# Kernel optimization log

Hardware: AMD Instinct MI355X
Metric: run time of the kernel (lower is better)

The kernel has to match this reference:

```python
import jax, jax.numpy as jnp
import numpy as np

CROP = (96.0, 192.0, 192.0)
SPACING = jnp.array([2.0, 1.0, 1.0], dtype=jnp.float32)
TOPK = 7
IGNORE_RATIO = 26
ALPHA, GAMMA = 0.75, 2.0
RATIO, NUM_HARD = 100, 100


def make_anchors(D, H, W):
    zz, yy, xx = jnp.meshgrid(jnp.arange(D, dtype=jnp.float32),
                              jnp.arange(H, dtype=jnp.float32),
                              jnp.arange(W, dtype=jnp.float32), indexing='ij')
    anchors = jnp.stack([zz, yy, xx], -1).reshape(-1, 3)  # [A,3] (z,y,x), z-major like cartesian_prod
    stride = jnp.array([CROP[0] / D, CROP[1] / H, CROP[2] / W], dtype=jnp.float32)
    return anchors, stride


def target_preprocess(ann):
    # ann [B,N,7] = (cz,cy,cx,d,h,w,label); clip boxes to the crop, keep boxes with
    c, s, label = ann[..., 0:3], ann[..., 3:6], ann[..., 6]
    has_box = label > -1
    lo = jnp.maximum(c - s / 2, 0.0)
    hi = jnp.minimum(c + s / 2, jnp.array(CROP, dtype=ann.dtype))
    n = jnp.clip(hi - lo, 0.0)
    vol = n[..., 0] * n[..., 1] * n[..., 2]
    percent = vol / (s[..., 0] * s[..., 1] * s[..., 2])
    good = (percent > 0.1) & (vol >= 15.0)
    keep = has_box & (vol > 0) & good
    rejected = has_box & (vol > 0) & (~good)
    new_box = jnp.concatenate([lo + n / 2, n, jnp.zeros_like(label)[..., None]], -1)
    ann_new = jnp.where(keep[..., None], new_box, -1.0)
    return ann_new, lo, hi, rejected


def build_grid_ignore(lo, hi, rejected, D, H, W):
    # Faithful to original: image-space coords index the feature grid directly,
    # with python-slice clipping emulated by the < / >= comparisons.
    def axis_mask(a0, a1, L):
        idx = jnp.arange(L, dtype=jnp.float32)
        return (idx >= jnp.floor(a0)[..., None]) & (idx < jnp.ceil(a1)[..., None])
    mz = axis_mask(lo[..., 0], hi[..., 0], D)  # [B,N,D]
    my = axis_mask(lo[..., 1], hi[..., 1], H)
    mx = axis_mask(lo[..., 2], hi[..., 2], W)
    region = (rejected[..., None, None, None] & mz[:, :, :, None, None]
              & my[:, :, None, :, None] & mx[:, :, None, None, :])
    return -jnp.any(region, axis=1).astype(jnp.float32)  # [B,D,H,W], 0 or -1


def scatter_count(inds, A):
    # one_hot(inds).sum(-2) without materializing [B,N,K,A]
    B, N, K = inds.shape
    bi = jnp.arange(B)[:, None, None]
    ni = jnp.arange(N)[None, :, None]
    return jnp.zeros((B, N, A), jnp.float32).at[bi, ni, inds].add(1.0)


def get_pos_target(ann, anchors, stride):
    B, N, _ = ann.shape
    A = anchors.shape[0]
    mask_gt = (ann[..., -1] > -1).astype(jnp.float32)  # [B,N]
    ctr = ann[..., :3] / stride
    half = ann[..., 3:6] / 2
    dist = -(((ctr[:, :, None, :] - anchors[None, None]) * SPACING) ** 2).sum(-1)  # [B,N,A]
    _, inds = jax.lax.top_k(dist, (IGNORE_RATIO + 1) * TOPK)
    mask_topk = scatter_count(inds[..., :TOPK], A)
    mask_ign = -scatter_count(inds[..., TOPK:], A)
    mask_pos = mask_topk * mask_gt[..., None]
    mask_ign = mask_ign * mask_gt[..., None]
    gt_idx = jnp.argmax(mask_pos, axis=1) + jnp.arange(B)[:, None] * N  # [B,A]
    t_ctr = ctr.reshape(-1, 3)[gt_idx]
    t_offset = t_ctr - anchors[None]
    t_shape = half.reshape(-1, 3)[gt_idx]
    t_bboxes = ann[..., :6].reshape(-1, 6)[gt_idx]
    t_scores = mask_pos.max(axis=1)[..., None]   # [B,A,1]
    m_ignore = mask_ign.min(axis=1)[..., None]
    return t_offset, t_shape, t_bboxes, t_scores, m_ignore


def bbox_diou(box1, box2, eps=1e-7):
    c1, s1 = box1[..., :3], box1[..., 3:]
    c2, s2 = box2[..., :3], box2[..., 3:]
    lo1, hi1 = c1 - s1 / 2, c1 + s1 / 2
    lo2, hi2 = c2 - s2 / 2, c2 + s2 / 2
    inter = jnp.clip(jnp.minimum(hi1, hi2) - jnp.maximum(lo1, lo2), 0.0).prod(-1) + eps
    union = s1.prod(-1) + s2.prod(-1) - inter
    iou = inter / union
    c2d = ((jnp.maximum(hi1, hi2) - jnp.minimum(lo1, lo2)) ** 2).sum(-1) + eps
    rho2 = (((lo2 + hi2) - (lo1 + hi1)) ** 2).sum(-1) / 4
    return iou - rho2 / c2d


def focal_cls_loss(pred, target, ignore):
    # pred/target/ignore: [B,A]. Hard-negative mining: top (100*num_pos) negatives
    # (or top 100 when no positives) via a rank mask over the descending sort.
    prob = jnp.clip(jax.nn.sigmoid(jax.lax.stop_gradient(pred)), 1e-4, 1.0 - 1e-4)
    is_pos = target == 1.0
    alpha_f = jnp.where(is_pos, ALPHA, 1.0 - ALPHA)
    fw = alpha_f * jnp.where(is_pos, 1.0 - prob, prob) ** GAMMA
    bce = jnp.logaddexp(0.0, pred) - pred * target  # BCE-with-logits, stable
    loss = jnp.where(ignore == 0, fw * bce, 0.0)
    loss = jnp.where((prob < 0.8) & is_pos, 4.0 * loss, loss)  # FN up-weighting
    npos = is_pos.sum(axis=1)
    pos_sum = jnp.where(is_pos, loss, 0.0).sum(axis=1)
    neg = jnp.where(target == 0.0, loss, -1.0)
    neg_sorted = jnp.flip(jnp.sort(neg, axis=1), axis=1)
    k = jnp.where(npos > 0, RATIO * npos, NUM_HARD)
    ranks = jnp.arange(neg.shape[1])[None, :]
    neg_sum = jnp.where((ranks < k[:, None]) & (neg_sorted >= 0), neg_sorted, 0.0).sum(axis=1)
    per_img = (pos_sum + neg_sum) / jnp.maximum(npos.astype(pred.dtype), 1.0)
    return per_img.mean()


def detection_loss(cls_out, shape_out, offset_out, annotations):
    B = cls_out.shape[0]
    D, H, W = cls_out.shape[2:]
    anchors, stride = make_anchors(D, H, W)
    pred_scores = cls_out.reshape(B, -1)                       # [B,A]
    pred_shapes = shape_out.reshape(B, 3, -1).transpose(0, 2, 1)   # [B,A,3]
    pred_offsets = offset_out.reshape(B, 3, -1).transpose(0, 2, 1)
    ann_new, lo, hi, rejected = target_preprocess(annotations)
    grid_ign = build_grid_ignore(lo, hi, rejected, D, H, W).reshape(B, -1)  # [B,A]
    pred_bboxes = jnp.concatenate([(anchors + pred_offsets) * stride, 2 * pred_shapes], -1)
    t_off, t_shape, t_bbox, t_scores, m_ign = get_pos_target(ann_new, anchors, stride)
    cls_l = focal_cls_loss(pred_scores, t_scores[..., 0], m_ign[..., 0] + grid_ign)
    fg = (t_scores[..., 0] == 1.0).astype(cls_out.dtype)  # [B,A]
    denom = jnp.maximum(fg.sum(), 1.0)
    shape_l = (jnp.abs(pred_shapes - t_shape) * fg[..., None]).sum() / (denom * 3)
    off_l = (jnp.abs(pred_offsets - t_off) * fg[..., None]).sum() / (denom * 3)
    iou_l = 1.0 - (bbox_diou(pred_bboxes, t_bbox) * fg).sum() / denom
    return cls_l, shape_l, off_l, iou_l


def setup_inputs() -> dict:
    key = jax.random.key(0)
    k1, k2, k3, k4, k5, k6 = jax.random.split(key, 6)
    B, N = 16, 8
    D, H, W = 24, 48, 48
    cls_out = jax.random.normal(k1, (B, 1, D, H, W), jnp.float32)
    shape_out = jax.random.uniform(k2, (B, 3, D, H, W), jnp.float32) * 4.0 + 1.0
    offset_out = jax.random.normal(k3, (B, 3, D, H, W), jnp.float32) * 0.5
    crop = jnp.array(CROP)
    ctr = jax.random.uniform(k4, (B, N, 3)) * (crop - 16.0) + 8.0
    size = jax.random.uniform(k5, (B, N, 3)) * 16.0 + 6.0
    size = size.at[:, 1, :].set(2.0)      # vol=8 < 15 -> rejected -> exercises ignore path
    ctr = ctr.at[:, 0, 0].set(3.0)        # near z=0 edge -> clipping path
    valid = jax.random.uniform(k6, (B, N)) < 0.6
    label = jnp.where(valid, 0.0, -1.0)
    annotations = jnp.where(valid[..., None],
                            jnp.concatenate([ctr, size, label[..., None]], -1), -1.0)
    return {"cls_out": cls_out, "shape_out": shape_out,
            "offset_out": offset_out, "annotations": annotations}


def reference(cls_out, shape_out, offset_out, annotations):
    return detection_loss(cls_out, shape_out, offset_out, annotations)
```

## Files before the change

### kernel.cpp

```cpp
#include <hip/hip_runtime.h>

#define BB 16
#define NN 8
#define DD 24
#define HH 48
#define WW 48
#define AA (DD*HH*WW)
#define AW (AA/32)
#define NSEG (AA/256)
#define TOPKc 7
#define KIGN 189
#define NB1 2048
#define DCAP 16384

#define WZC 13
#define WYC 25
#define WXC 25
#define WYXC (WYC*WXC)
#define CNTC (WZC*WYXC)
#define CPT 32

struct GT {
  float ctr[3];
  float half_[3];
  float bbox[6];
  float lo[3], hi[3];
  int keep, rejected;
};

struct Accum {
  int   npos[BB];
  float pos_sum[BB];
  float shape_sum, off_sum, iou_sum;
  int   B1[BB];
  int   cnt_above[BB];
  float per_img[BB];
};

__device__ __forceinline__ unsigned fkey(float f) {
  unsigned u = __float_as_uint(f);
  return (u & 0x80000000u) ? ~u : (u | 0x80000000u);
}
__device__ __forceinline__ float fkey_inv(unsigned k) {
  return __uint_as_float((k & 0x80000000u) ? (k & 0x7FFFFFFFu) : ~k);
}

__device__ __forceinline__ void agg_lds_add(int* h, int bin) {
  const int lane = threadIdx.x & 63;
  unsigned long long todo = __ballot(bin >= 0);
  while (todo) {
    const int leader = __ffsll((unsigned long long)todo) - 1;
    const int lbin = __shfl(bin, leader, 64);
    const unsigned long long eq = __ballot(bin == lbin) & todo;
    if (lane == leader) atomicAdd(&h[lbin], (int)__popcll(eq));
    todo &= ~eq;
  }
}

__device__ __forceinline__ GT prep_gt(const float* __restrict__ p) {
  const float cz=p[0], cy=p[1], cx=p[2], sz=p[3], sy=p[4], sx=p[5], label=p[6];
  const bool has_box = label > -1.0f;
  const float loz = fmaxf(cz - sz*0.5f, 0.0f);
  const float loy = fmaxf(cy - sy*0.5f, 0.0f);
  const float lox = fmaxf(cx - sx*0.5f, 0.0f);
  const float hiz = fminf(cz + sz*0.5f, 96.0f);
  const float hiy = fminf(cy + sy*0.5f, 192.0f);
  const float hix = fminf(cx + sx*0.5f, 192.0f);
  const float nz = fmaxf(hiz - loz, 0.0f);
  const float ny = fmaxf(hiy - loy, 0.0f);
  const float nx = fmaxf(hix - lox, 0.0f);
  const float vol = nz * ny * nx;
  const float percent = vol / (sz * sy * sx);
  const bool good = (percent > 0.1f) && (vol >= 15.0f);
  const bool keep = has_box && (vol > 0.0f) && good;
  const bool rejected = has_box && (vol > 0.0f) && !good;
  GT g;
  const float ncz = loz + nz*0.5f, ncy = loy + ny*0.5f, ncx = lox + nx*0.5f;
  if (keep) {
    g.ctr[0]=ncz*0.25f; g.ctr[1]=ncy*0.25f; g.ctr[2]=ncx*0.25f;
    g.half_[0]=nz*0.5f; g.half_[1]=ny*0.5f; g.half_[2]=nx*0.5f;
    g.bbox[0]=ncz; g.bbox[1]=ncy; g.bbox[2]=ncx;
    g.bbox[3]=nz;  g.bbox[4]=ny;  g.bbox[5]=nx;
  } else {
    for (int j=0;j<3;++j){ g.ctr[j]=-0.25f; g.half_[j]=-0.5f; }
    for (int j=0;j<6;++j) g.bbox[j]=-1.0f;
  }
  g.lo[0]=loz; g.lo[1]=loy; g.lo[2]=lox;
  g.hi[0]=hiz; g.hi[1]=hiy; g.hi[2]=hix;
  g.keep = keep ? 1 : 0;
  g.rejected = rejected ? 1 : 0;
  return g;
}

__device__ __forceinline__ int blockReduceSumI(int v) {
  __shared__ int s[4];
  for (int off = 32; off; off >>= 1) v += __shfl_down(v, off, 64);
  if ((threadIdx.x & 63) == 0) s[threadIdx.x >> 6] = v;
  __syncthreads();
  int r = s[0] + s[1] + s[2] + s[3];
  __syncthreads();
  return r;
}
__device__ __forceinline__ float blockReduceSumF(float v) {
  __shared__ float s[4];
  for (int off = 32; off; off >>= 1) v += __shfl_down(v, off, 64);
  if ((threadIdx.x & 63) == 0) s[threadIdx.x >> 6] = v;
  __syncthreads();
  float r = s[0] + s[1] + s[2] + s[3];
  __syncthreads();
  return r;
}
__device__ __forceinline__ int redI1024(int v) {
  __shared__ int s[16];
  for (int off = 32; off; off >>= 1) v += __shfl_down(v, off, 64);
  if ((threadIdx.x & 63) == 0) s[threadIdx.x >> 6] = v;
  __syncthreads();
  int r = 0;
  #pragma unroll
  for (int w = 0; w < 16; ++w) r += s[w];
  __syncthreads();
  return r;
}
__device__ __forceinline__ float redF1024(float v) {
  __shared__ float s[16];
  for (int off = 32; off; off >>= 1) v += __shfl_down(v, off, 64);
  if ((threadIdx.x & 63) == 0) s[threadIdx.x >> 6] = v;
  __syncthreads();
  float r = 0.0f;
  #pragma unroll
  for (int w = 0; w < 16; ++w) r += s[w];
  __syncthreads();
  return r;
}

__device__ void suffix_find_1024(const int* h, int nbins, int ktarget,
                                 int* s_bin, int* s_cnt) {
  const int tid = threadIdx.x, lane = tid & 63, wave = tid >> 6;
  const int C = nbins >> 10;
  int csum = 0;
  for (int i = 0; i < C; ++i) csum += h[tid*C + i];
  __shared__ int wt[16];
  int S = csum;
  #pragma unroll
  for (int off = 1; off < 64; off <<= 1) {
    const int t = __shfl_down(S, off, 64);
    if (lane + off < 64) S += t;
  }
  if (lane == 0) wt[wave] = S;
  __syncthreads();
  int above = 0;
  for (int w = wave + 1; w < 16; ++w) above += wt[w];
  const int sfx = above + (S - csum);
  if (sfx < ktarget && sfx + csum >= ktarget) {
    int running = sfx;
    for (int i = C - 1; i >= 0; --i) {
      const int c = h[tid*C + i];
      if (running + c >= ktarget) { *s_bin = tid*C + i; *s_cnt = running; break; }
      running += c;
    }
  }
  __syncthreads();
}

__device__ __forceinline__ float seg_load(const float* lb, const int* pfi,
                                          const int* cn, int i) {
  int lo = 0, hi = NSEG - 1;
  while (lo < hi) { const int mid = (lo + hi) >> 1; if (pfi[mid] > i) hi = mid; else lo = mid + 1; }
  return lb[lo*256 + (i - (pfi[lo] - cn[lo]))];
}

#define N_POS4  (BB*AA/4)
#define N_IGN4  (BB*AW/4)
#define N_HIST4 (BB*NB1/4)

__global__ __launch_bounds__(256) void k0_init(int4* pos_n4, uint4* ign4,
                                               int4* hist4, Accum* acc) {
  const int idx = blockIdx.x*256 + threadIdx.x;
  if (idx < N_POS4) {
    pos_n4[idx] = make_int4(0x7FFFFFFF,0x7FFFFFFF,0x7FFFFFFF,0x7FFFFFFF);
  } else if (idx < N_POS4 + N_IGN4) {
    ign4[idx - N_POS4] = make_uint4(0,0,0,0);
  } else if (idx < N_POS4 + N_IGN4 + N_HIST4) {
    hist4[idx - (N_POS4 + N_IGN4)] = make_int4(0,0,0,0);
  }
  if (idx < BB) {
    acc->npos[idx] = 0; acc->pos_sum[idx] = 0.0f;
    acc->B1[idx] = 0; acc->cnt_above[idx] = 0;
  }
  if (idx == 0) { acc->shape_sum = 0.0f; acc->off_sum = 0.0f; acc->iou_sum = 0.0f; }
}

__global__ __launch_bounds__(256) void k2_topk(const float* __restrict__ ann,
                                               int* __restrict__ pos_n,
                                               unsigned* __restrict__ ign) {
  const int bn = blockIdx.x;
  const int b = bn >> 3, n = bn & 7;
  const GT g = prep_gt(ann + bn*7);
  if (!g.keep) return;
  const float cz = g.ctr[0], cy = g.ctr[1], cx = g.ctr[2];
  const int rz = (int)floorf(cz + 0.5f);
  const int ry = (int)floorf(cy + 0.5f);
  const int rx = (int)floorf(cx + 0.5f);
  const int zlo = min(max(rz - 6, 0),  DD - WZC);
  const int ylo = min(max(ry - 12, 0), HH - WYC);
  const int xlo = min(max(rx - 12, 0), WW - WXC);
  const int tid = threadIdx.x;

  __shared__ int h[1024];
  #pragma unroll
  for (int i = 0; i < 4; ++i) h[tid + i*256] = 0;
  __syncthreads();

#define K2_KEYAID(J, KEY, AID, VALID)                                   \
  const int ci = tid + (J)*256;                                         \
  const bool VALID = ci < CNTC;                                         \
  const int wz = ci / WYXC;                                             \
  const int rem = ci - wz*WYXC;                                         \
  const int wy = rem / WXC;                                             \
  const int wx = rem - wy*WXC;                                          \
  const int z = zlo + wz, y = ylo + wy, x = xlo + wx;                   \
  const float dz = (cz - (float)z) * 2.0f;                              \
  const float dy = cy - (float)y;                                       \
  const float dx = cx - (float)x;                                      \
  const unsigned KEY = fkey(-__builtin_fmaf(dz, dz, __builtin_fmaf(dy, dy, dx*dx))); \
  const int AID = (z*HH + y)*WW + x;

  #pragma unroll
  for (int j = 0; j < CPT; ++j) {
    K2_KEYAID(j, key, aid, valid)
    (void)aid;
    if (valid) atomicAdd(&h[key >> 21], 1);
  }
  __syncthreads();

  __shared__ int wt[4];
  __shared__ int sB7, sA7, sB9, sA9;
  const int lane = tid & 63, wave = tid >> 6;
  int csum = 0;
  #pragma unroll
  for (int i = 0; i < 4; ++i) csum += h[tid*4 + i];
  int Ssc = csum;
  #pragma unroll
  for (int off = 1; off < 64; off <<= 1) {
    const int t = __shfl_down(Ssc, off, 64);
    if (lane + off < 64) Ssc += t;
  }
  if (lane == 0) wt[wave] = Ssc;
  __syncthreads();
  int above = 0;
  for (int w = wave + 1; w < 4; ++w) above += wt[w];
  const int sfx = above + (Ssc - csum);
  if (sfx < TOPKc && sfx + csum >= TOPKc) {
    int run = sfx;
    for (int i = 3; i >= 0; --i) {
      const int c = h[tid*4 + i];
      if (run + c >= TOPKc) { sB7 = tid*4 + i; sA7 = run; break; }
      run += c;
    }
  }
  if (sfx < KIGN && sfx + csum >= KIGN) {
    int run = sfx;
    for (int i = 3; i >= 0; --i) {
      const int c = h[tid*4 + i];
      if (run + c >= KIGN) { sB9 = tid*4 + i; sA9 = run; break; }
      run += c;
    }
  }
  __syncthreads();
  const int B7 = sB7, A7 = sA7, B9 = sB9, A9 = sA9;

  __shared__ unsigned kl7[512], kl9[512];
  __shared__ int n7s, n9s;
  if (tid == 0) { n7s = 0; n9s = 0; }
  __syncthreads();
  #pragma unroll
  for (int j = 0; j < CPT; ++j) {
    K2_KEYAID(j, key, aid, valid)
    (void)aid;
    if (valid) {
      const int bin = (int)(key >> 21);
      if (bin == B7) { const int p = atomicAdd(&n7s, 1); if (p < 512) kl7[p] = key; }
      if (bin == B9 && B9 != B7) { const int p = atomicAdd(&n9s, 1); if (p < 512) kl9[p] = key; }
    }
  }
  __syncthreads();

  __shared__ unsigned sk7, sk9;
  __shared__ int scg7, scg9;
  const int T7c = min(n7s, 512), T9c = min(n9s, 512);
  for (int i = tid; i < T7c; i += 256) {
    const unsigned xv = kl7[i];
    int gt = 0, eq = 0;
    for (int j2 = 0; j2 < T7c; ++j2) { gt += (kl7[j2] > xv); eq += (kl7[j2] == xv); }
    if (A7 + gt < TOPKc && TOPKc <= A7 + gt + eq) { sk7 = xv; scg7 = A7 + gt; }
    if (B9 == B7 && A7 + gt < KIGN && KIGN <= A7 + gt + eq) { sk9 = xv; scg9 = A7 + gt; }
  }
  if (B9 != B7) {
    for (int i = tid; i < T9c; i += 256) {
      const unsigned xv = kl9[i];
      int gt = 0, eq = 0;
      for (int j2 = 0; j2 < T9c; ++j2) { gt += (kl9[j2] > xv); eq += (kl9[j2] == xv); }
      if (A9 + gt < KIGN && KIGN <= A9 + gt + eq) { sk9 = xv; scg9 = A9 + gt; }
    }
  }
  __syncthreads();
  const unsigned k7 = sk7, k9 = sk9;
  const int cg7 = scg7, cg9 = scg9;

  __shared__ int tc7, tc9;
  __shared__ int tl7[256], tr7[256], tl9[256], tr9[256];
  if (tid == 0) { tc7 = 0; tc9 = 0; }
  __syncthreads();
  #pragma unroll
  for (int j = 0; j < CPT; ++j) {
    K2_KEYAID(j, key, aid, valid)
    if (valid) {
      if (key == k7) { const int p = atomicAdd(&tc7, 1); if (p < 256) tl7[p] = aid; }
      if (key == k9 && k9 != k7) { const int p = atomicAdd(&tc9, 1); if (p < 256) tl9[p] = aid; }
    }
  }
  __syncthreads();
  const int T7 = min(tc7, 256), T9 = min(tc9, 256);
  for (int i = tid; i < T7; i += 256) {
    const int ai = tl7[i]; int r = 0;
    for (int j2 = 0; j2 < T7; ++j2) r += (tl7[j2] < ai);
    tr7[i] = r;
  }
  for (int i = tid; i < T9; i += 256) {
    const int ai = tl9[i]; int r = 0;
    for (int j2 = 0; j2 < T9; ++j2) r += (tl9[j2] < ai);
    tr9[i] = r;
  }
  __syncthreads();

  int* pb = pos_n + (size_t)b*AA;
  unsigned* ib = ign + (size_t)b*AW;
  #pragma unroll
  for (int j = 0; j < CPT; ++j) {
    K2_KEYAID(j, key, aid, valid)
    if (valid) {
      bool top = false, igf = false;
      if (key > k7) top = true;
      else if (key == k7) {
        int r = 0;
        for (int t = 0; t < T7; ++t) if (tl7[t] == aid) r = tr7[t];
        const int ov = cg7 + r;
        if (ov < TOPKc) top = true;
        else if (ov < KIGN) igf = true;
      } else if (key > k9) igf = true;
      else if (key == k9) {
        int r = 0;
        for (int t = 0; t < T9; ++t) if (tl9[t] == aid) r = tr9[t];
        if (cg9 + r < KIGN) igf = true;
      }
      if (top) atomicMin(&pb[aid], n);
      else if (igf) atomicOr(&ib[aid >> 5], 1u << (aid & 31));
    }
  }
#undef K2_KEYAID
}

__global__ __launch_bounds__(256) void k3_loss(
    const float* __restrict__ cls_out, const float* __restrict__ shape_out,
    const float* __restrict__ offset_out, const float* __restrict__ ann,
    const int* __restrict__ pos_n, const unsigned* __restrict__ ignm,
    float* __restrict__ neg, int* __restrict__ ghist, Accum* acc) {
  __shared__ GT sg[NN];
  __shared__ int h1[NB1];
  const int idx = blockIdx.x * 256 + threadIdx.x;
  const int b = idx / AA;
  const int a = idx - b * AA;
  if (threadIdx.x < NN) sg[threadIdx.x] = prep_gt(ann + (b*NN + threadIdx.x)*7);
  #pragma unroll
  for (int i = 0; i < NB1/256; ++i) h1[threadIdx.x + i*256] = 0;
  __syncthreads();
  const int z = a / (HH*WW);
  const int rr = a - z*(HH*WW);
  const int y = rr / WW;
  const int x = rr - y*WW;

  float gign = 0.0f;
  for (int n = 0; n < NN; ++n) {
    if (!sg[n].rejected) continue;
    if ((float)z >= floorf(sg[n].lo[0]) && (float)z < ceilf(sg[n].hi[0]) &&
        (float)y >= floorf(sg[n].lo[1]) && (float)y < ceilf(sg[n].hi[1]) &&
        (float)x >= floorf(sg[n].lo[2]) && (float)x < ceilf(sg[n].hi[2])) gign = -1.0f;
  }

  const int pn = pos_n[idx];
  const bool is_pos = (pn < NN);
  const float target = is_pos ? 1.0f : 0.0f;
  const int ibit = (ignm[b*AW + (a >> 5)] >> (a & 31)) & 1;
  const float ignore = (ibit ? -1.0f : 0.0f) + gign;
  const float pred = cls_out[idx];
  float prob = 1.0f / (1.0f + expf(-pred));
  prob = fminf(fmaxf(prob, 1e-4f), 1.0f - 1e-4f);
  const float alpha_f = is_pos ? 0.75f : 0.25f;
  const float pt = is_pos ? (1.0f - prob) : prob;
  const float fw = alpha_f * pt * pt;
  const float bce = fmaxf(pred, 0.0f) + log1pf(expf(-fabsf(pred))) - pred * target;
  float loss = (ignore == 0.0f) ? fw * bce : 0.0f;
  if (prob < 0.8f && is_pos) loss *= 4.0f;
  const float nval = is_pos ? -1.0f : loss;
  neg[idx] = nval;

  agg_lds_add(h1, (int)(fkey(nval) >> 21));

  const int np = blockReduceSumI(is_pos ? 1 : 0);
  const float ps = blockReduceSumF(is_pos ? loss : 0.0f);
  if (threadIdx.x == 0 && np) {
    atomicAdd(&acc->npos[b], np);
    atomicAdd(&acc->pos_sum[b], ps);
  }

  if (is_pos) {
    const GT& g = sg[pn];
    const float toz = g.ctr[0] - (float)z;
    const float toy = g.ctr[1] - (float)y;
    const float tox = g.ctr[2] - (float)x;
    const float poz = offset_out[((size_t)b*3 + 0)*AA + a];
    const float poy = offset_out[((size_t)b*3 + 1)*AA + a];
    const float pox = offset_out[((size_t)b*3 + 2)*AA + a];
    const float psz = shape_out[((size_t)b*3 + 0)*AA + a];
    const float psy = shape_out[((size_t)b*3 + 1)*AA + a];
    const float psx = shape_out[((size_t)b*3 + 2)*AA + a];
    const float off_t = fabsf(poz - toz) + fabsf(poy - toy) + fabsf(pox - tox);
    const float shp_t = fabsf(psz - g.half_[0]) + fabsf(psy - g.half_[1]) + fabsf(psx - g.half_[2]);
    const float c1z = ((float)z + poz) * 4.0f;
    const float c1y = ((float)y + poy) * 4.0f;
    const float c1x = ((float)x + pox) * 4.0f;
    const float s1z = 2.0f*psz, s1y = 2.0f*psy, s1x = 2.0f*psx;
    const float lo1z = c1z - s1z*0.5f, hi1z = c1z + s1z*0.5f;
    const float lo1y = c1y - s1y*0.5f, hi1y = c1y + s1y*0.5f;
    const float lo1x = c1x - s1x*0.5f, hi1x = c1x + s1x*0.5f;
    const float c2z = g.bbox[0], c2y = g.bbox[1], c2x = g.bbox[2];
    const float s2z = g.bbox[3], s2y = g.bbox[4], s2x = g.bbox[5];
    const float lo2z = c2z - s2z*0.5f, hi2z = c2z + s2z*0.5f;
    const float lo2y = c2y - s2y*0.5f, hi2y = c2y + s2y*0.5f;
    const float lo2x = c2x - s2x*0.5f, hi2x = c2x + s2x*0.5f;
    const float iz = fmaxf(fminf(hi1z,hi2z) - fmaxf(lo1z,lo2z), 0.0f);
    const float iy = fmaxf(fminf(hi1y,hi2y) - fmaxf(lo1y,lo2y), 0.0f);
    const float ix = fmaxf(fminf(hi1x,hi2x) - fmaxf(lo1x,lo2x), 0.0f);
    const float inter = iz*iy*ix + 1e-7f;
    const float uni = s1z*s1y*s1x + s2z*s2y*s2x - inter;
    const float iou = inter / uni;
    const float ez = fmaxf(hi1z,hi2z) - fminf(lo1z,lo2z);
    const float ey = fmaxf(hi1y,hi2y) - fminf(lo1y,lo2y);
    const float ex = fmaxf(hi1x,hi2x) - fminf(lo1x,lo2x);
    const float c2d = (ez*ez + ey*ey) + ex*ex + 1e-7f;
    const float rz2 = (lo2z + hi2z) - (lo1z + hi1z);
    const float ry2 = (lo2y + hi2y) - (lo1y + hi1y);
    const float rx2 = (lo2x + hi2x) - (lo1x + hi1x);
    const float rho2 = ((rz2*rz2 + ry2*ry2) + rx2*rx2) * 0.25f;
    const float diou = iou - rho2 / c2d;
    atomicAdd(&acc->shape_sum, shp_t);
    atomicAdd(&acc->off_sum, off_t);
    atomicAdd(&acc->iou_sum, diou);
  }

  __syncthreads();
  #pragma unroll
  for (int i = 0; i < NB1/256; ++i) {
    const int bin = threadIdx.x + i*256;
    const int c = h1[bin];
    if (c) atomicAdd(&ghist[b*NB1 + bin], c);
  }
}

__global__ __launch_bounds__(256) void ks1(const int* __restrict__ ghist, Accum* acc) {
  const int b = blockIdx.x;
  const int* hb = ghist + b*NB1;
  const int tid = threadIdx.x, lane = tid & 63, wave = tid >> 6;
  const int npos = acc->npos[b];
  const int k = npos > 0 ? 100*npos : 100;
  int csum = 0;
  #pragma unroll
  for (int i = 0; i < 8; ++i) csum += hb[tid*8 + i];
  __shared__ int wt[4];
  int S = csum;
  #pragma unroll
  for (int off = 1; off < 64; off <<= 1) {
    const int t = __shfl_down(S, off, 64);
    if (lane + off < 64) S += t;
  }
  if (lane == 0) wt[wave] = S;
  __syncthreads();
  int above = 0;
  for (int w = wave + 1; w < 4; ++w) above += wt[w];
  const int sfx = above + (S - csum);
  if (sfx < k && sfx + csum >= k) {
    int running = sfx;
    for (int i = 7; i >= 0; --i) {
      const int c = hb[tid*8 + i];
      if (running + c >= k) {
        acc->B1[b] = tid*8 + i;
        acc->cnt_above[b] = running;
        break;
      }
      running += c;
    }
  }
}

__global__ __launch_bounds__(256) void kgather(const float* __restrict__ neg,
                                               float* __restrict__ list,
                                               float* __restrict__ psum,
                                               int* __restrict__ seg_cnt,
                                               const Accum* __restrict__ acc) {
  const int idx = blockIdx.x*256 + threadIdx.x;
  const int b = idx / AA;
  const int seg = (idx - b*AA) >> 8;
  const int tid = threadIdx.x, lane = tid & 63, wave = tid >> 6;
  const int B1 = acc->B1[b];
  const float val = neg[idx];
  const int bin = (int)(fkey(val) >> 21);
  const float aval = (bin > B1 && bin >= 1024) ? val : 0.0f;
  const float bs = blockReduceSumF(aval);

  const bool match = (bin == B1);
  const unsigned long long mask = __ballot(match);
  __shared__ int wc[4];
  if (lane == 0) wc[wave] = (int)__popcll(mask);
  __syncthreads();
  int wbase = 0;
  for (int w = 0; w < wave; ++w) wbase += wc[w];
  if (match) {
    const int pos = (int)__popcll(mask & ((1ull << lane) - 1ull));
    list[(size_t)b*AA + seg*256 + wbase + pos] = val;
  }
  if (tid == 0) {
    psum[b*NSEG + seg] = bs;
    seg_cnt[b*NSEG + seg] = wc[0] + wc[1] + wc[2] + wc[3];
  }
}

__global__ __launch_bounds__(1024) void ksel(const float* __restrict__ list,
                                             const float* __restrict__ psum,
                                             const int* __restrict__ seg_cnt,
                                             Accum* acc) {
  const int b = blockIdx.x;
  const int tid = threadIdx.x;
  const int npos = acc->npos[b];
  const int k = npos > 0 ? 100*npos : 100;
  const int B1 = acc->B1[b];
  const float pos_sum = acc->pos_sum[b];

  const float pv = (tid < NSEG) ? psum[b*NSEG + tid] : 0.0f;
  const float sum_above = redF1024(pv);

  if (B1 < 1024) {
    if (tid == 0) acc->per_img[b] = (pos_sum + sum_above) / fmaxf((float)npos, 1.0f);
    return;
  }

  __shared__ int cn[NSEG];
  __shared__ int pfi[256];
  if (tid < 256) {
    const int c = (tid < NSEG) ? seg_cnt[b*NSEG + tid] : 0;
    if (tid < NSEG) cn[tid] = c;
    pfi[tid] = c;
  }
  __syncthreads();
  for (int off = 1; off < 256; off <<= 1) {
    int v = 0;
    if (tid < 256 && tid >= off) v = pfi[tid - off];
    __syncthreads();
    if (tid < 256) pfi[tid] += v;
    __syncthreads();
  }
  const int S = pfi[NSEG - 1];
  const int cnt_above = acc->cnt_above[b];
  const int kt2 = k - cnt_above;
  const float* lb = list + (size_t)b*AA;

  __shared__ float ld[DCAP];
  const bool fits = (S <= DCAP);
  if (fits) {
    for (int i = tid; i < S; i += 1024) ld[i] = seg_load(lb, pfi, cn, i);
  }
  __syncthreads();

  __shared__ int h[2048];
  __shared__ int sB2, sC2, sB3, sC3;
  h[tid] = 0; h[tid + 1024] = 0;
  __syncthreads();
  for (int i0 = 0; i0 < S; i0 += 1024) {
    const int i = i0 + tid;
    if (i < S) {
      const float v = fits ? ld[i] : seg_load(lb, pfi, cn, i);
      atomicAdd(&h[(fkey(v) >> 10) & 0x7FF], 1);
    }
  }
  __syncthreads();
  suffix_find_1024(h, 2048, kt2, &sB2, &sC2);
  const int B2 = sB2;
  const int kt3 = kt2 - sC2;
  h[tid < 1024 ? tid : 0] = (tid < 1024) ? 0 : h[0];
  __syncthreads();
  float msum = 0.0f; int mcnt = 0;
  for (int i0 = 0; i0 < S; i0 += 1024) {
    const int i = i0 + tid;
    if (i < S) {
      const float v = fits ? ld[i] : seg_load(lb, pfi, cn, i);
      const unsigned key = fkey(v);
      const int sub = (int)((key >> 10) & 0x7FF);
      if (sub > B2) { msum += v; mcnt++; }
      else if (sub == B2) atomicAdd(&h[key & 0x3FF], 1);
    }
  }
  __syncthreads();
  suffix_find_1024(h, 1024, kt3, &sB3, &sC3);
  const int B3 = sB3;
  const unsigned Kstar = ((unsigned)B1 << 21) | ((unsigned)B2 << 10) | (unsigned)B3;
  const float v = fkey_inv(Kstar);
  for (int i0 = 0; i0 < S; i0 += 1024) {
    const int i = i0 + tid;
    if (i < S) {
      const float x = fits ? ld[i] : seg_load(lb, pfi, cn, i);
      const unsigned key = fkey(x);
      if ((int)((key >> 10) & 0x7FF) == B2 && (int)(key & 0x3FF) > B3) { msum += x; mcnt++; }
    }
  }
  const int cg = redI1024(mcnt);
  const float sg = redF1024(msum);
  if (tid == 0) {
    const int total_gt = cnt_above + cg;
    const float ns = sum_above + sg + (float)(k - total_gt) * v;
    acc->per_img[b] = (pos_sum + ns) / fmaxf((float)npos, 1.0f);
  }
}

__global__ void k5_final(const Accum* __restrict__ acc, float* __restrict__ out) {
  float s = 0.0f; int tot = 0;
  for (int b = 0; b < BB; ++b) { s += acc->per_img[b]; tot += acc->npos[b]; }
  out[0] = s / (float)BB;
  const float denom = fmaxf((float)tot, 1.0f);
  out[1] = acc->shape_sum / (denom * 3.0f);
  out[2] = acc->off_sum / (denom * 3.0f);
  out[3] = 1.0f - acc->iou_sum / denom;
}

extern "C" void kernel_launch(void* const* d_in, const int* in_sizes, int n_in,
                              void* d_out, int out_size, void* d_ws, size_t ws_size,
                              hipStream_t stream) {
  const float* cls_out    = (const float*)d_in[0];
  const float* shape_out  = (const float*)d_in[1];
  const float* offset_out = (const float*)d_in[2];
  const float* ann        = (const float*)d_in[3];
  float* out = (float*)d_out;

  char* ws = (char*)d_ws;
  Accum* acc    = (Accum*)ws;
  int* pos_n    = (int*)(ws + 1024);
  unsigned* ign = (unsigned*)(pos_n + (size_t)BB*AA);
  float* neg    = (float*)(ign + (size_t)BB*AW);
  int* ghist    = (int*)(neg + (size_t)BB*AA);
  float* psum   = (float*)(ghist + (size_t)BB*NB1);
  int* seg_cnt  = (int*)(psum + (size_t)BB*NSEG);
  float* list   = (float*)pos_n;

  const int n0 = N_POS4 + N_IGN4 + N_HIST4;
  hipLaunchKernelGGL(k0_init, dim3(n0/256), dim3(256), 0, stream,
                     (int4*)pos_n, (uint4*)ign, (int4*)ghist, acc);
  hipLaunchKernelGGL(k2_topk, dim3(BB*NN), dim3(256), 0, stream, ann, pos_n, ign);
  hipLaunchKernelGGL(k3_loss, dim3((BB*AA)/256), dim3(256), 0, stream,
                     cls_out, shape_out, offset_out, ann, pos_n, ign, neg, ghist, acc);
  hipLaunchKernelGGL(ks1, dim3(BB), dim3(256), 0, stream, ghist, acc);
  hipLaunchKernelGGL(kgather, dim3((BB*AA)/256), dim3(256), 0, stream,
                     neg, list, psum, seg_cnt, acc);
  hipLaunchKernelGGL(ksel, dim3(BB), dim3(1024), 0, stream, list, psum, seg_cnt, acc);
  hipLaunchKernelGGL(k5_final, dim3(1), dim3(1), 0, stream, acc, out);
}
```

Measured before the change: 69.60 us.

## Replace dense positive map with compact top-k lists and fold small kernels

Instead of a dense per-anchor int map initialised to sentinel and written with atomicMin, each GT now records its up-to-7 top-k anchors in a small list, and the loss kernel scans that 56-entry list from shared memory to decide positives. This removes a full BB*AA init write and read. The histogram threshold kernel ks1 is folded into each kgather block, which recomputes it redundantly. The final reduction k5 is folded into ksel through a last-block-done counter. Net effect is fewer launches and less memory traffic, at the cost of a 56-way compare per anchor and repeated histogram scans.

```diff
diff --git a/kernel.cpp b/kernel.cpp
--- a/kernel.cpp
+++ b/kernel.cpp
@@ -8,6 +8,7 @@
 #define AA (DD*HH*WW)
 #define AW (AA/32)
 #define NSEG (AA/256)
+#define NBLK ((BB*AA)/256)
 #define TOPKc 7
 #define KIGN 189
 #define NB1 2048
@@ -32,9 +33,11 @@
   int   npos[BB];
   float pos_sum[BB];
   float shape_sum, off_sum, iou_sum;
+  float sum_above[BB];
   int   B1[BB];
   int   cnt_above[BB];
   float per_img[BB];
+  int   done;
 };
 
 __device__ __forceinline__ unsigned fkey(float f) {
@@ -169,32 +172,22 @@
   return lb[lo*256 + (i - (pfi[lo] - cn[lo]))];
 }
 
-#define N_POS4  (BB*AA/4)
-#define N_IGN4  (BB*AW/4)
-#define N_HIST4 (BB*NB1/4)
-
-__global__ __launch_bounds__(256) void k0_init(int4* pos_n4, uint4* ign4,
-                                               int4* hist4, Accum* acc) {
+__global__ __launch_bounds__(256) void k0_init(unsigned* ign, int* ghist,
+                                               int* plist, Accum* acc) {
   const int idx = blockIdx.x*256 + threadIdx.x;
-  if (idx < N_POS4) {
-    pos_n4[idx] = make_int4(0x7FFFFFFF,0x7FFFFFFF,0x7FFFFFFF,0x7FFFFFFF);
-  } else if (idx < N_POS4 + N_IGN4) {
-    ign4[idx - N_POS4] = make_uint4(0,0,0,0);
-  } else if (idx < N_POS4 + N_IGN4 + N_HIST4) {
-    hist4[idx - (N_POS4 + N_IGN4)] = make_int4(0,0,0,0);
-  }
-  if (idx < BB) {
-    acc->npos[idx] = 0; acc->pos_sum[idx] = 0.0f;
-    acc->B1[idx] = 0; acc->cnt_above[idx] = 0;
-  }
-  if (idx == 0) { acc->shape_sum = 0.0f; acc->off_sum = 0.0f; acc->iou_sum = 0.0f; }
+  if (idx < BB*AW) ign[idx] = 0u;
+  const int i2 = idx - BB*AW;
+  if (i2 >= 0 && i2 < BB*NB1) ghist[i2] = 0;
+  const int i3 = idx - BB*AW - BB*NB1;
+  if (i3 >= 0 && i3 < BB*NN*TOPKc) plist[i3] = -1;
+  if (idx < (int)(sizeof(Accum)/4)) ((int*)acc)[idx] = 0;
 }
 
 __global__ __launch_bounds__(256) void k2_topk(const float* __restrict__ ann,
-                                               int* __restrict__ pos_n,
+                                               int* __restrict__ plist,
                                                unsigned* __restrict__ ign) {
   const int bn = blockIdx.x;
-  const int b = bn >> 3, n = bn & 7;
+  const int b = bn >> 3;
   const GT g = prep_gt(ann + bn*7);
   if (!g.keep) return;
   const float cz = g.ctr[0], cy = g.ctr[1], cx = g.ctr[2];
@@ -331,9 +324,10 @@
     for (int j2 = 0; j2 < T9; ++j2) r += (tl9[j2] < ai);
     tr9[i] = r;
   }
-  __syncthreads();
-
-  int* pb = pos_n + (size_t)b*AA;
+  __shared__ int pcnt;
+  if (tid == 0) pcnt = 0;
+  __syncthreads();
+
   unsigned* ib = ign + (size_t)b*AW;
   #pragma unroll
   for (int j = 0; j < CPT; ++j) {
@@ -353,7 +347,7 @@
         for (int t = 0; t < T9; ++t) if (tl9[t] == aid) r = tr9[t];
         if (cg9 + r < KIGN) igf = true;
       }
-      if (top) atomicMin(&pb[aid], n);
+      if (top) { const int s = atomicAdd(&pcnt, 1); if (s < TOPKc) plist[bn*TOPKc + s] = aid; }
       else if (igf) atomicOr(&ib[aid >> 5], 1u << (aid & 31));
     }
   }
@@ -363,14 +357,16 @@
 __global__ __launch_bounds__(256) void k3_loss(
     const float* __restrict__ cls_out, const float* __restrict__ shape_out,
     const float* __restrict__ offset_out, const float* __restrict__ ann,
-    const int* __restrict__ pos_n, const unsigned* __restrict__ ignm,
+    const int* __restrict__ plist, const unsigned* __restrict__ ignm,
     float* __restrict__ neg, int* __restrict__ ghist, Accum* acc) {
   __shared__ GT sg[NN];
+  __shared__ int pl[NN*TOPKc];
   __shared__ int h1[NB1];
   const int idx = blockIdx.x * 256 + threadIdx.x;
   const int b = idx / AA;
   const int a = idx - b * AA;
   if (threadIdx.x < NN) sg[threadIdx.x] = prep_gt(ann + (b*NN + threadIdx.x)*7);
+  if (threadIdx.x < NN*TOPKc) pl[threadIdx.x] = plist[b*NN*TOPKc + threadIdx.x];
   #pragma unroll
   for (int i = 0; i < NB1/256; ++i) h1[threadIdx.x + i*256] = 0;
   __syncthreads();
@@ -387,7 +383,9 @@
         (float)x >= floorf(sg[n].lo[2]) && (float)x < ceilf(sg[n].hi[2])) gign = -1.0f;
   }
 
-  const int pn = pos_n[idx];
+  int pn = NN;
+  #pragma unroll
+  for (int j = NN*TOPKc - 1; j >= 0; --j) if (pl[j] == a) pn = j / TOPKc;
   const bool is_pos = (pn < NN);
   const float target = is_pos ? 1.0f : 0.0f;
   const int ibit = (ignm[b*AW + (a >> 5)] >> (a & 31)) & 1;
@@ -467,51 +465,53 @@
   }
 }
 
-__global__ __launch_bounds__(256) void ks1(const int* __restrict__ ghist, Accum* acc) {
-  const int b = blockIdx.x;
-  const int* hb = ghist + b*NB1;
-  const int tid = threadIdx.x, lane = tid & 63, wave = tid >> 6;
-  const int npos = acc->npos[b];
-  const int k = npos > 0 ? 100*npos : 100;
-  int csum = 0;
-  #pragma unroll
-  for (int i = 0; i < 8; ++i) csum += hb[tid*8 + i];
-  __shared__ int wt[4];
-  int S = csum;
-  #pragma unroll
-  for (int off = 1; off < 64; off <<= 1) {
-    const int t = __shfl_down(S, off, 64);
-    if (lane + off < 64) S += t;
-  }
-  if (lane == 0) wt[wave] = S;
-  __syncthreads();
-  int above = 0;
-  for (int w = wave + 1; w < 4; ++w) above += wt[w];
-  const int sfx = above + (S - csum);
-  if (sfx < k && sfx + csum >= k) {
-    int running = sfx;
-    for (int i = 7; i >= 0; --i) {
-      const int c = hb[tid*8 + i];
-      if (running + c >= k) {
-        acc->B1[b] = tid*8 + i;
-        acc->cnt_above[b] = running;
-        break;
-      }
-      running += c;
-    }
-  }
-}
-
 __global__ __launch_bounds__(256) void kgather(const float* __restrict__ neg,
+                                               const int* __restrict__ ghist,
                                                float* __restrict__ list,
                                                float* __restrict__ psum,
                                                int* __restrict__ seg_cnt,
-                                               const Accum* __restrict__ acc) {
-  const int idx = blockIdx.x*256 + threadIdx.x;
-  const int b = idx / AA;
-  const int seg = (idx - b*AA) >> 8;
+                                               Accum* acc) {
+  const int bid = blockIdx.x;
   const int tid = threadIdx.x, lane = tid & 63, wave = tid >> 6;
-  const int B1 = acc->B1[b];
+  const int b = bid / NSEG;
+  const int seg = bid - b*NSEG;
+
+  const int npos = acc->npos[b];
+  const int k = npos > 0 ? 100*npos : 100;
+  __shared__ int sB1, sCA;
+  {
+    const int* hb = ghist + b*NB1;
+    int hv[8];
+    #pragma unroll
+    for (int i = 0; i < 8; ++i) hv[i] = hb[tid*8 + i];
+    int csum = 0;
+    #pragma unroll
+    for (int i = 0; i < 8; ++i) csum += hv[i];
+    __shared__ int wt[4];
+    int S = csum;
+    #pragma unroll
+    for (int off = 1; off < 64; off <<= 1) {
+      const int t = __shfl_down(S, off, 64);
+      if (lane + off < 64) S += t;
+    }
+    if (lane == 0) wt[wave] = S;
+    __syncthreads();
+    int above = 0;
+    for (int w = wave + 1; w < 4; ++w) above += wt[w];
+    const int sfx = above + (S - csum);
+    if (sfx < k && sfx + csum >= k) {
+      int run = sfx;
+      for (int i = 7; i >= 0; --i) {
+        if (run + hv[i] >= k) { sB1 = tid*8 + i; sCA = run; break; }
+        run += hv[i];
+      }
+    }
+    __syncthreads();
+  }
+  const int B1 = sB1, cnt_above = sCA;
+  if (seg == 0 && tid == 0) { acc->B1[b] = B1; acc->cnt_above[b] = cnt_above; }
+
+  const int idx = b*AA + seg*256 + tid;
   const float val = neg[idx];
   const int bin = (int)(fkey(val) >> 21);
   const float aval = (bin > B1 && bin >= 1024) ? val : 0.0f;
@@ -529,15 +529,15 @@
     list[(size_t)b*AA + seg*256 + wbase + pos] = val;
   }
   if (tid == 0) {
-    psum[b*NSEG + seg] = bs;
-    seg_cnt[b*NSEG + seg] = wc[0] + wc[1] + wc[2] + wc[3];
+    psum[bid] = bs;
+    seg_cnt[bid] = wc[0] + wc[1] + wc[2] + wc[3];
   }
 }
 
 __global__ __launch_bounds__(1024) void ksel(const float* __restrict__ list,
                                              const float* __restrict__ psum,
                                              const int* __restrict__ seg_cnt,
-                                             Accum* acc) {
+                                             Accum* acc, float* __restrict__ out) {
   const int b = blockIdx.x;
   const int tid = threadIdx.x;
   const int npos = acc->npos[b];
@@ -550,94 +550,99 @@
 
   if (B1 < 1024) {
     if (tid == 0) acc->per_img[b] = (pos_sum + sum_above) / fmaxf((float)npos, 1.0f);
-    return;
-  }
-
-  __shared__ int cn[NSEG];
-  __shared__ int pfi[256];
-  if (tid < 256) {
-    const int c = (tid < NSEG) ? seg_cnt[b*NSEG + tid] : 0;
-    if (tid < NSEG) cn[tid] = c;
-    pfi[tid] = c;
-  }
-  __syncthreads();
-  for (int off = 1; off < 256; off <<= 1) {
-    int v = 0;
-    if (tid < 256 && tid >= off) v = pfi[tid - off];
-    __syncthreads();
-    if (tid < 256) pfi[tid] += v;
-    __syncthreads();
-  }
-  const int S = pfi[NSEG - 1];
-  const int cnt_above = acc->cnt_above[b];
-  const int kt2 = k - cnt_above;
-  const float* lb = list + (size_t)b*AA;
-
-  __shared__ float ld[DCAP];
-  const bool fits = (S <= DCAP);
-  if (fits) {
-    for (int i = tid; i < S; i += 1024) ld[i] = seg_load(lb, pfi, cn, i);
-  }
-  __syncthreads();
-
-  __shared__ int h[2048];
-  __shared__ int sB2, sC2, sB3, sC3;
-  h[tid] = 0; h[tid + 1024] = 0;
-  __syncthreads();
-  for (int i0 = 0; i0 < S; i0 += 1024) {
-    const int i = i0 + tid;
-    if (i < S) {
-      const float v = fits ? ld[i] : seg_load(lb, pfi, cn, i);
-      atomicAdd(&h[(fkey(v) >> 10) & 0x7FF], 1);
-    }
-  }
-  __syncthreads();
-  suffix_find_1024(h, 2048, kt2, &sB2, &sC2);
-  const int B2 = sB2;
-  const int kt3 = kt2 - sC2;
-  h[tid < 1024 ? tid : 0] = (tid < 1024) ? 0 : h[0];
-  __syncthreads();
-  float msum = 0.0f; int mcnt = 0;
-  for (int i0 = 0; i0 < S; i0 += 1024) {
-    const int i = i0 + tid;
-    if (i < S) {
-      const float v = fits ? ld[i] : seg_load(lb, pfi, cn, i);
-      const unsigned key = fkey(v);
-      const int sub = (int)((key >> 10) & 0x7FF);
-      if (sub > B2) { msum += v; mcnt++; }
-      else if (sub == B2) atomicAdd(&h[key & 0x3FF], 1);
-    }
-  }
-  __syncthreads();
-  suffix_find_1024(h, 1024, kt3, &sB3, &sC3);
-  const int B3 = sB3;
-  const unsigned Kstar = ((unsigned)B1 << 21) | ((unsigned)B2 << 10) | (unsigned)B3;
-  const float v = fkey_inv(Kstar);
-  for (int i0 = 0; i0 < S; i0 += 1024) {
-    const int i = i0 + tid;
-    if (i < S) {
-      const float x = fits ? ld[i] : seg_load(lb, pfi, cn, i);
-      const unsigned key = fkey(x);
-      if ((int)((key >> 10) & 0x7FF) == B2 && (int)(key & 0x3FF) > B3) { msum += x; mcnt++; }
-    }
-  }
-  const int cg = redI1024(mcnt);
-  const float sg = redF1024(msum);
+  } else {
+    __shared__ int cn[NSEG];
+    __shared__ int pfi[256];
+    if (tid < 256) {
+      const int c = (tid < NSEG) ? seg_cnt[b*NSEG + tid] : 0;
+      if (tid < NSEG) cn[tid] = c;
+      pfi[tid] = c;
+    }
+    __syncthreads();
+    for (int off = 1; off < 256; off <<= 1) {
+      int v = 0;
+      if (tid < 256 && tid >= off) v = pfi[tid - off];
+      __syncthreads();
+      if (tid < 256) pfi[tid] += v;
+      __syncthreads();
+    }
+    const int S = pfi[NSEG - 1];
+    const int cnt_above = acc->cnt_above[b];
+    const int kt2 = k - cnt_above;
+    const float* lb = list + (size_t)b*AA;
+
+    __shared__ float ld[DCAP];
+    const bool fits = (S <= DCAP);
+    if (fits) {
+      for (int i = tid; i < S; i += 1024) ld[i] = seg_load(lb, pfi, cn, i);
+    }
+    __syncthreads();
+
+    __shared__ int h[2048];
+    __shared__ int sB2, sC2, sB3, sC3;
+    h[tid] = 0; h[tid + 1024] = 0;
+    __syncthreads();
+    for (int i0 = 0; i0 < S; i0 += 1024) {
+      const int i = i0 + tid;
+      if (i < S) {
+        const float v = fits ? ld[i] : seg_load(lb, pfi, cn, i);
+        atomicAdd(&h[(fkey(v) >> 10) & 0x7FF], 1);
+      }
+    }
+    __syncthreads();
+    suffix_find_1024(h, 2048, kt2, &sB2, &sC2);
+    const int B2 = sB2;
+    const int kt3 = kt2 - sC2;
+    if (tid < 1024) h[tid] = 0;
+    __syncthreads();
+    float msum = 0.0f; int mcnt = 0;
+    for (int i0 = 0; i0 < S; i0 += 1024) {
+      const int i = i0 + tid;
+      if (i < S) {
+        const float v = fits ? ld[i] : seg_load(lb, pfi, cn, i);
+        const unsigned key = fkey(v);
+        const int sub = (int)((key >> 10) & 0x7FF);
+        if (sub > B2) { msum += v; mcnt++; }
+        else if (sub == B2) atomicAdd(&h[key & 0x3FF], 1);
+      }
+    }
+    __syncthreads();
+    suffix_find_1024(h, 1024, kt3, &sB3, &sC3);
+    const int B3 = sB3;
+    const unsigned Kstar = ((unsigned)B1 << 21) | ((unsigned)B2 << 10) | (unsigned)B3;
+    const float vK = fkey_inv(Kstar);
+    for (int i0 = 0; i0 < S; i0 += 1024) {
+      const int i = i0 + tid;
+      if (i < S) {
+        const float x = fits ? ld[i] : seg_load(lb, pfi, cn, i);
+        const unsigned key = fkey(x);
+        if ((int)((key >> 10) & 0x7FF) == B2 && (int)(key & 0x3FF) > B3) { msum += x; mcnt++; }
+      }
+    }
+    const int cg = redI1024(mcnt);
+    const float sg = redF1024(msum);
+    if (tid == 0) {
+      const int total_gt = acc->cnt_above[b] + cg;
+      const float ns = sum_above + sg + (float)(k - total_gt) * vK;
+      acc->per_img[b] = (pos_sum + ns) / fmaxf((float)npos, 1.0f);
+    }
+  }
+
+  __threadfence();
+  __shared__ int isLast;
+  if (tid == 0) isLast = (atomicAdd(&acc->done, 1) == BB - 1) ? 1 : 0;
+  __syncthreads();
+  if (!isLast) return;
+  __threadfence();
   if (tid == 0) {
-    const int total_gt = cnt_above + cg;
-    const float ns = sum_above + sg + (float)(k - total_gt) * v;
-    acc->per_img[b] = (pos_sum + ns) / fmaxf((float)npos, 1.0f);
-  }
-}
-
-__global__ void k5_final(const Accum* __restrict__ acc, float* __restrict__ out) {
-  float s = 0.0f; int tot = 0;
-  for (int b = 0; b < BB; ++b) { s += acc->per_img[b]; tot += acc->npos[b]; }
-  out[0] = s / (float)BB;
-  const float denom = fmaxf((float)tot, 1.0f);
-  out[1] = acc->shape_sum / (denom * 3.0f);
-  out[2] = acc->off_sum / (denom * 3.0f);
-  out[3] = 1.0f - acc->iou_sum / denom;
+    float s = 0.0f; int tot = 0;
+    for (int b2 = 0; b2 < BB; ++b2) { s += acc->per_img[b2]; tot += acc->npos[b2]; }
+    out[0] = s / (float)BB;
+    const float denom = fmaxf((float)tot, 1.0f);
+    out[1] = acc->shape_sum / (denom * 3.0f);
+    out[2] = acc->off_sum / (denom * 3.0f);
+    out[3] = 1.0f - acc->iou_sum / denom;
+  }
 }
 
 extern "C" void kernel_launch(void* const* d_in, const int* in_sizes, int n_in,
@@ -651,23 +656,22 @@
 
   char* ws = (char*)d_ws;
   Accum* acc    = (Accum*)ws;
-  int* pos_n    = (int*)(ws + 1024);
-  unsigned* ign = (unsigned*)(pos_n + (size_t)BB*AA);
-  float* neg    = (float*)(ign + (size_t)BB*AW);
-  int* ghist    = (int*)(neg + (size_t)BB*AA);
-  float* psum   = (float*)(ghist + (size_t)BB*NB1);
+  unsigned* ign = (unsigned*)(ws + 1024);
+  int* ghist    = (int*)(ign + (size_t)BB*AW);
+  int* plist    = (int*)(ghist + (size_t)BB*NB1);
+  float* neg    = (float*)(plist + (size_t)BB*NN*TOPKc);
+  float* list   = neg + (size_t)BB*AA;
+  float* psum   = list + (size_t)BB*AA;
   int* seg_cnt  = (int*)(psum + (size_t)BB*NSEG);
-  float* list   = (float*)pos_n;
-
-  const int n0 = N_POS4 + N_IGN4 + N_HIST4;
-  hipLaunchKernelGGL(k0_init, dim3(n0/256), dim3(256), 0, stream,
-                     (int4*)pos_n, (uint4*)ign, (int4*)ghist, acc);
-  hipLaunchKernelGGL(k2_topk, dim3(BB*NN), dim3(256), 0, stream, ann, pos_n, ign);
-  hipLaunchKernelGGL(k3_loss, dim3((BB*AA)/256), dim3(256), 0, stream,
-                     cls_out, shape_out, offset_out, ann, pos_n, ign, neg, ghist, acc);
-  hipLaunchKernelGGL(ks1, dim3(BB), dim3(256), 0, stream, ghist, acc);
-  hipLaunchKernelGGL(kgather, dim3((BB*AA)/256), dim3(256), 0, stream,
-                     neg, list, psum, seg_cnt, acc);
-  hipLaunchKernelGGL(ksel, dim3(BB), dim3(1024), 0, stream, list, psum, seg_cnt, acc);
-  hipLaunchKernelGGL(k5_final, dim3(1), dim3(1), 0, stream, acc, out);
-}
+
+  const int n0 = BB*AW + BB*NB1 + BB*NN*TOPKc;
+  hipLaunchKernelGGL(k0_init, dim3((n0 + 255)/256), dim3(256), 0, stream,
+                     ign, ghist, plist, acc);
+  hipLaunchKernelGGL(k2_topk, dim3(BB*NN), dim3(256), 0, stream, ann, plist, ign);
+  hipLaunchKernelGGL(k3_loss, dim3(NBLK), dim3(256), 0, stream,
+                     cls_out, shape_out, offset_out, ann, plist, ign, neg, ghist, acc);
+  hipLaunchKernelGGL(kgather, dim3(NBLK), dim3(256), 0, stream,
+                     neg, ghist, list, psum, seg_cnt, acc);
+  hipLaunchKernelGGL(ksel, dim3(BB), dim3(1024), 0, stream,
+                     list, psum, seg_cnt, acc, out);
+}
```

After: 78.41 us. 12.7% more time.
